# Kernel tuning notes

Measured on AMD Instinct MI355X. Metric: run time of the kernel, lower is better.

## Reference

```python
import jax, jax.numpy as jnp
from jax import lax
import numpy as np

NUM_CLASSES = 81
SCALES = (64.0, 128.0, 256.0)
RATIOS = (0.5, 1.0, 2.0)
A = 9                       # anchors per cell = len(SCALES)*len(RATIOS)
POOL = 14
PRE_NMS = 6000
PROPOSAL_COUNT = 1000
NMS_THR = 0.7
BN_EPS = 1e-3               # keras BatchNormalization default epsilon
NEG = -1e9                  # suppressed-score sentinel (avoids -inf NaNs in grad)


def conv(x, w, b, padding):
    return lax.conv_general_dilated(x, w, (1, 1), padding,
        dimension_numbers=('NHWC', 'HWIO', 'NHWC')) + b


def bn(x, g, b, m, v):
    # inference-mode batch norm
    return (x - m) * (g / jnp.sqrt(v + BN_EPS)) + b


def generate_anchors(fh, fw, H, W):
    sy, sx = H / fh, W / fw
    scales = jnp.asarray(SCALES, jnp.float32)
    sq = jnp.sqrt(jnp.asarray(RATIOS, jnp.float32))
    ah = (scales[:, None] * sq[None, :]).reshape(-1)   # [A]
    aw = (scales[:, None] / sq[None, :]).reshape(-1)
    cy = (jnp.arange(fh, dtype=jnp.float32) + 0.5) * sy
    cx = (jnp.arange(fw, dtype=jnp.float32) + 0.5) * sx
    cy, cx = jnp.meshgrid(cy, cx, indexing='ij')
    cy, cx = cy[..., None], cx[..., None]              # [fh,fw,1]
    # (y1, x1, y2, x2), flattened per-cell-then-anchor to match channel layout
    return jnp.stack([cy - ah / 2, cx - aw / 2, cy + ah / 2, cx + aw / 2], -1).reshape(-1, 4)


def decode(anchors, deltas):
    h = anchors[:, 2] - anchors[:, 0]
    w = anchors[:, 3] - anchors[:, 1]
    cy = anchors[:, 0] + 0.5 * h + deltas[:, 0] * h
    cx = anchors[:, 1] + 0.5 * w + deltas[:, 1] * w
    h = h * jnp.exp(deltas[:, 2])
    w = w * jnp.exp(deltas[:, 3])
    return jnp.stack([cy - 0.5 * h, cx - 0.5 * w, cy + 0.5 * h, cx + 0.5 * w], 1)


def iou_one_vs_all(box, boxes):
    y1 = jnp.maximum(box[0], boxes[:, 0]); x1 = jnp.maximum(box[1], boxes[:, 1])
    y2 = jnp.minimum(box[2], boxes[:, 2]); x2 = jnp.minimum(box[3], boxes[:, 3])
    inter = jnp.maximum(y2 - y1, 0.0) * jnp.maximum(x2 - x1, 0.0)
    a = (box[2] - box[0]) * (box[3] - box[1])
    b = (boxes[:, 2] - boxes[:, 0]) * (boxes[:, 3] - boxes[:, 1])
    return inter / (a + b - inter + 1e-8)


def nms(boxes, scores, max_out, thr):
    # greedy NMS with fixed iteration count (jit-friendly)
    def step(s, _):
        i = jnp.argmax(s)
        valid = s[i] > NEG * 0.5
        sup = iou_one_vs_all(boxes[i], boxes) > thr
        s = jnp.where(sup, NEG, s).at[i].set(NEG)
        return s, (i, valid)
    _, (idx, valid) = lax.scan(step, scores, None, length=max_out)
    return idx, valid


def roi_align(feat, boxes):
    # feat: [H, W, C]; boxes: [N, 4] normalized (y1, x1, y2, x2)
    H, W, _ = feat.shape
    t = jnp.arange(POOL, dtype=jnp.float32) / (POOL - 1)
    def one(box):
        y1, x1, y2, x2 = box
        ys = (y1 + t * (y2 - y1)) * (H - 1)
        xs = (x1 + t * (x2 - x1)) * (W - 1)
        y0 = jnp.clip(jnp.floor(ys), 0, H - 2).astype(jnp.int32)
        x0 = jnp.clip(jnp.floor(xs), 0, W - 2).astype(jnp.int32)
        wy = jnp.clip(ys - y0, 0.0, 1.0)[:, None, None]
        wx = jnp.clip(xs - x0, 0.0, 1.0)[None, :, None]
        r0, r1 = feat[y0], feat[y0 + 1]                    # [P, W, C]
        top = r0[:, x0] * (1 - wx) + r0[:, x0 + 1] * wx    # [P, P, C]
        bot = r1[:, x0] * (1 - wx) + r1[:, x0 + 1] * wx
        return top * (1 - wy) + bot * wy
    return jax.vmap(one)(boxes)                            # [N, P, P, C]


def setup_inputs() -> dict:
    key = jax.random.key(0)
    ks = jax.random.split(key, 12)
    f = lambda k, shp, s=0.02: jax.random.normal(k, shp, jnp.float32) * s
    C_in, C_fpn, C_rpn = 1024, 256, 512
    return dict(
        feature=jax.random.normal(ks[0], (1, 64, 64, C_in), jnp.float32),
        w_fpn1=f(ks[1], (1, 1, C_in, C_fpn)), b_fpn1=jnp.zeros((C_fpn,), jnp.float32),
        w_fpn2=f(ks[2], (3, 3, C_fpn, C_fpn)), b_fpn2=jnp.zeros((C_fpn,), jnp.float32),
        w_rpn=f(ks[3], (3, 3, C_fpn, C_rpn)), b_rpn=jnp.zeros((C_rpn,), jnp.float32),
        w_cls=f(ks[4], (1, 1, C_rpn, A * 2)), b_cls=jnp.zeros((A * 2,), jnp.float32),
        w_dlt=f(ks[5], (1, 1, C_rpn, A * 4)), b_dlt=jnp.zeros((A * 4,), jnp.float32),
        w_rc1=f(ks[6], (POOL, POOL, C_fpn, 1024), 0.005), b_rc1=jnp.zeros((1024,), jnp.float32),
        g1=jnp.ones((1024,), jnp.float32), be1=jnp.zeros((1024,), jnp.float32),
        m1=jnp.zeros((1024,), jnp.float32), v1=jnp.ones((1024,), jnp.float32),
        w_rc2=f(ks[7], (1024, 1024)), b_rc2=jnp.zeros((1024,), jnp.float32),
        g2=jnp.ones((1024,), jnp.float32), be2=jnp.zeros((1024,), jnp.float32),
        m2=jnp.zeros((1024,), jnp.float32), v2=jnp.ones((1024,), jnp.float32),
        w_log=f(ks[8], (1024, NUM_CLASSES)), b_log=jnp.zeros((NUM_CLASSES,), jnp.float32),
        w_bfc=f(ks[9], (1024, NUM_CLASSES * 4)), b_bfc=jnp.zeros((NUM_CLASSES * 4,), jnp.float32),
        image_h=512, image_w=512,
    )


def reference(feature, w_fpn1, b_fpn1, w_fpn2, b_fpn2, w_rpn, b_rpn, w_cls, b_cls,
              w_dlt, b_dlt, w_rc1, b_rc1, g1, be1, m1, v1, w_rc2, b_rc2, g2, be2,
              m2, v2, w_log, b_log, w_bfc, b_bfc, image_h, image_w):
    H, W = float(image_h), float(image_w)
    # ---- FPN neck: 1x1 then 3x3 conv to 256ch ----
    x = conv(feature, w_fpn1, b_fpn1, 'VALID')
    x = conv(x, w_fpn2, b_fpn2, 'SAME')                # [1, fh, fw, 256]
    fh, fw = x.shape[1], x.shape[2]
    # ---- RPN head ----
    shared = jax.nn.relu(conv(x, w_rpn, b_rpn, 'SAME'))
    rpn_logits = conv(shared, w_cls, b_cls, 'VALID').reshape(-1, 2)
    rpn_probs = jax.nn.softmax(rpn_logits, axis=-1)    # [num_anchors, 2]
    rpn_deltas = conv(shared, w_dlt, b_dlt, 'VALID').reshape(-1, 4)
    # ---- proposal generation: anchors -> top-k -> decode -> clip -> NMS ----
    anchors = generate_anchors(fh, fw, H, W)
    scores = rpn_probs[:, 1]
    k = min(PRE_NMS, anchors.shape[0])
    top_scores, ix = lax.top_k(scores, k)
    props = decode(anchors[ix], rpn_deltas[ix])
    window = jnp.asarray([H, W, H, W], jnp.float32)
    props = jnp.minimum(jnp.maximum(props, 0.0), window)   # bbox_clip
    props = props / window                                  # normalize
    sel, valid = nms(props, top_scores, PROPOSAL_COUNT, NMS_THR)
    proposals = props[sel] * valid[:, None].astype(props.dtype)  # [1000, 4]
    # ---- RoI pooling + RCNN head ----
    rois = roi_align(x[0], proposals)                       # [1000, 14, 14, 256]
    h1 = rois.reshape(PROPOSAL_COUNT, -1) @ w_rc1.reshape(-1, 1024) + b_rc1
    h1 = jax.nn.relu(bn(h1, g1, be1, m1, v1))
    h2 = jax.nn.relu(bn(h1 @ w_rc2 + b_rc2, g2, be2, m2, v2))
    cls_probs = jax.nn.softmax(h2 @ w_log + b_log, axis=-1)         # [1000, 81]
    box_deltas = (h2 @ w_bfc + b_bfc).reshape(-1, NUM_CLASSES, 4)   # [1000, 81, 4]
    return (rpn_probs.reshape(1, -1, 2), rpn_deltas.reshape(1, -1, 4),
            proposals, cls_probs, box_deltas)
```

## Files before the change

kernel.cpp:

```cpp
#include <hip/hip_runtime.h>
#include <hip/hip_bf16.h>

typedef unsigned int u32;
typedef unsigned long long u64;
typedef unsigned short u16;

typedef float f32x4 __attribute__((ext_vector_type(4)));
typedef __bf16 bf16x8 __attribute__((ext_vector_type(8)));
typedef unsigned short u16x8 __attribute__((ext_vector_type(8)));
typedef unsigned short u16x4 __attribute__((ext_vector_type(4)));

#define NA 36864
#define PRE_NMS 6000
#define NPROP 1000
#define KROI 50176
#define MASKW 94
#define MASKT_STRIDE 6144
#define KSPLIT 8
#define KCHUNK (KROI / KSPLIT)
#define BN_EPS 1e-3f
#define CONV_TILES 3136

__device__ __forceinline__ u16 f2bf(float v) {
    __bf16 h = (__bf16)v;
    return __builtin_bit_cast(u16, h);
}
__device__ __forceinline__ bf16x8 ldfrag(const u16* p) {
    return __builtin_bit_cast(bf16x8, *(const u16x8*)p);
}
__device__ __forceinline__ void gload16(const void* g, void* l) {
    __builtin_amdgcn_global_load_lds(
        (const __attribute__((address_space(1))) unsigned int*)g,
        (__attribute__((address_space(3))) unsigned int*)l, 16, 0, 0);
}

template <bool CONV3>
__global__ __launch_bounds__(128) void gemm_v3(
    const float* __restrict__ A, const float* __restrict__ B, float* __restrict__ part,
    int M, int N, int K, int kchunk) {
    __shared__ float As[2][16][132];
    __shared__ float Bs[2][16][68];
    const int tid = threadIdx.x;
    const int bm = blockIdx.x * 128, bn = blockIdx.y * 64;
    const int ks = blockIdx.z;
    const int kbeg = ks * kchunk, kend = kbeg + kchunk;
    const int tx = tid & 7, ty = tid >> 3;
    (void)K;

    float4 ra[4], rb[2];
    auto loadA = [&](int k0, int i) -> float4 {
        int e = tid + 128 * i;
        int m = e >> 2, kq = (e & 3) * 4;
        float4 v = {0.f, 0.f, 0.f, 0.f};
        int gm = bm + m;
        if (CONV3) {
            int gg = k0 >> 8;
            int dy = gg / 3, dx = gg - 3 * dy;
            int pr = gm >> 6, pc = gm & 63;
            int sr = pr + dy - 1, sc = pc + dx - 1;
            int ch = (k0 & 255) + kq;
            if (sr >= 0 && sr < 64 && sc >= 0 && sc < 64)
                v = *(const float4*)&A[(size_t)((sr << 6) + sc) * 256 + ch];
        } else {
            if (gm < M) v = *(const float4*)&A[(size_t)gm * K + k0 + kq];
        }
        return v;
    };
    auto loadB = [&](int k0, int i) -> float4 {
        int e = tid + 128 * i;
        int n4 = (e & 15) * 4, kk = e >> 4;
        return *(const float4*)&B[(size_t)(k0 + kk) * N + bn + n4];
    };
    auto stage = [&](int s) {
#pragma unroll
        for (int i = 0; i < 4; ++i) {
            int e = tid + 128 * i; int m = e >> 2, kq = (e & 3) * 4;
            As[s][kq + 0][m] = ra[i].x; As[s][kq + 1][m] = ra[i].y;
            As[s][kq + 2][m] = ra[i].z; As[s][kq + 3][m] = ra[i].w;
        }
#pragma unroll
        for (int i = 0; i < 2; ++i) {
            int e = tid + 128 * i; int n4 = (e & 15) * 4, kk = e >> 4;
            *(float4*)&Bs[s][kk][n4] = rb[i];
        }
    };

    float acc[8][8] = {};
#pragma unroll
    for (int i = 0; i < 4; ++i) ra[i] = loadA(kbeg, i);
#pragma unroll
    for (int i = 0; i < 2; ++i) rb[i] = loadB(kbeg, i);
    stage(0);
    if (kbeg + 16 < kend) {
#pragma unroll
        for (int i = 0; i < 4; ++i) ra[i] = loadA(kbeg + 16, i);
#pragma unroll
        for (int i = 0; i < 2; ++i) rb[i] = loadB(kbeg + 16, i);
    }
    __syncthreads();
    int s = 0;
    for (int k0 = kbeg; k0 < kend; k0 += 16) {
        if (k0 + 16 < kend) {
            stage(s ^ 1);
            if (k0 + 32 < kend) {
#pragma unroll
                for (int i = 0; i < 4; ++i) ra[i] = loadA(k0 + 32, i);
#pragma unroll
                for (int i = 0; i < 2; ++i) rb[i] = loadB(k0 + 32, i);
            }
        }
#pragma unroll
        for (int kk = 0; kk < 16; ++kk) {
            float4 a0 = *(const float4*)&As[s][kk][8 * ty];
            float4 a1 = *(const float4*)&As[s][kk][8 * ty + 4];
            float4 b0 = *(const float4*)&Bs[s][kk][8 * tx];
            float4 b1 = *(const float4*)&Bs[s][kk][8 * tx + 4];
            const float av[8] = {a0.x, a0.y, a0.z, a0.w, a1.x, a1.y, a1.z, a1.w};
            const float bv[8] = {b0.x, b0.y, b0.z, b0.w, b1.x, b1.y, b1.z, b1.w};
#pragma unroll
            for (int r = 0; r < 8; ++r)
#pragma unroll
                for (int c = 0; c < 8; ++c) acc[r][c] = fmaf(av[r], bv[c], acc[r][c]);
        }
        __syncthreads();
        s ^= 1;
    }
    float* P = part + (size_t)ks * ((size_t)M * N);
#pragma unroll
    for (int r = 0; r < 8; ++r) {
        int gm = bm + 8 * ty + r;
        if (gm >= M) continue;
        *(float4*)&P[(size_t)gm * N + bn + 8 * tx] = *(const float4*)&acc[r][0];
        *(float4*)&P[(size_t)gm * N + bn + 8 * tx + 4] = *(const float4*)&acc[r][4];
    }
}

template <int EPI>
__global__ __launch_bounds__(256) void reduce_part(
    const float* __restrict__ part, float* __restrict__ C, int M, int N, int KS,
    const float* __restrict__ bias, const float* __restrict__ g,
    const float* __restrict__ be, const float* __restrict__ mu,
    const float* __restrict__ var) {
    int i = blockIdx.x * 256 + threadIdx.x;
    int total = (M * N) >> 2;
    if (i >= total) return;
    size_t off = (size_t)i * 4;
    int n = (int)(off % (size_t)N);
    size_t slice = (size_t)M * N;
    float4 sv = {0.f, 0.f, 0.f, 0.f};
    for (int k = 0; k < KS; ++k) {
        float4 v = *(const float4*)&part[(size_t)k * slice + off];
        sv.x += v.x; sv.y += v.y; sv.z += v.z; sv.w += v.w;
    }
    float o[4] = {sv.x, sv.y, sv.z, sv.w};
#pragma unroll
    for (int j = 0; j < 4; ++j) {
        float v = o[j] + bias[n + j];
        if constexpr (EPI == 1) v = fmaxf(v, 0.f);
        if constexpr (EPI == 2) {
            float sc = g[n + j] / sqrtf(var[n + j] + BN_EPS);
            v = (v - mu[n + j]) * sc + be[n + j];
            v = fmaxf(v, 0.f);
        }
        o[j] = v;
    }
    *(float4*)&C[off] = *(const float4*)&o[0];
}

__global__ __launch_bounds__(256) void pack_heads(
    const float* __restrict__ wc, const float* __restrict__ wd,
    const float* __restrict__ bc, const float* __restrict__ bd,
    float* __restrict__ wCat, float* __restrict__ bCat) {
    int i = blockIdx.x * 256 + threadIdx.x;
    if (i < 512 * 64) {
        int k = i >> 6, n = i & 63;
        float v = 0.f;
        if (n < 18) v = wc[k * 18 + n];
        else if (n < 54) v = wd[k * 36 + (n - 18)];
        wCat[i] = v;
    }
    if (i < 64) bCat[i] = (i < 18) ? bc[i] : ((i < 54) ? bd[i - 18] : 0.f);
}

__global__ __launch_bounds__(256) void pack_roi_heads(
    const float* __restrict__ wl, const float* __restrict__ wb,
    const float* __restrict__ bl, const float* __restrict__ bb,
    float* __restrict__ wH, float* __restrict__ bH) {
    int i = blockIdx.x * 256 + threadIdx.x;
    if (i < 1024 * 512) {
        int k = i >> 9, n = i & 511;
        float v = 0.f;
        if (n < 81) v = wl[k * 81 + n];
        else if (n < 405) v = wb[k * 324 + (n - 81)];
        wH[i] = v;
    }
    if (i < 512) bH[i] = (i < 81) ? bl[i] : ((i < 405) ? bb[i - 81] : 0.f);
}

__global__ __launch_bounds__(256) void split_roi(
    const float* __restrict__ hr, float* __restrict__ out4) {
    int i = blockIdx.x * 256 + threadIdx.x;
    if (i >= NPROP * 324) return;
    int r = i / 324, c = i - r * 324;
    out4[i] = hr[r * 512 + 81 + c];
}

__global__ __launch_bounds__(256) void rpn_probs_keys(
    const float* __restrict__ hc, float* __restrict__ out0, float* __restrict__ out1,
    u64* __restrict__ keys) {
    int i = blockIdx.x * 256 + threadIdx.x;
    if (i >= NA) return;
    int cell = i / 9, a = i - cell * 9;
    const float* row = &hc[cell * 64];
    float l0 = row[2 * a], l1 = row[2 * a + 1];
    float m = fmaxf(l0, l1);
    float e0 = expf(l0 - m), e1 = expf(l1 - m);
    float ssum = e0 + e1;
    float p0 = e0 / ssum, p1 = e1 / ssum;
    out0[2 * i] = p0;
    out0[2 * i + 1] = p1;
    keys[i] = ((u64)__float_as_uint(p1) << 32) | (u64)(0xFFFFFFFFu - (u32)i);
    const float* src = row + 18 + 4 * a;
    float4 d = {src[0], src[1], src[2], src[3]};
    *(float4*)&out1[(size_t)i * 4] = d;
}

__global__ __launch_bounds__(1024) void radix_select_compact(
    const u64* __restrict__ keys, u64* __restrict__ skeys) {
    __shared__ u32 hist[256];
    __shared__ u64 sPrefix, sMask;
    __shared__ int sRank;
    __shared__ u32 sCount;
    int tid = threadIdx.x;
    if (tid == 0) { sPrefix = 0; sMask = 0; sRank = PRE_NMS; sCount = 0; }
    __syncthreads();
    for (int p = 56; p >= 0; p -= 8) {
        if (tid < 256) hist[tid] = 0;
        __syncthreads();
        u64 pref = sPrefix, msk = sMask;
        for (int i = tid; i < NA; i += 1024) {
            u64 k = keys[i];
            if ((k & msk) == pref) atomicAdd(&hist[(u32)((k >> p) & 255)], 1u);
        }
        __syncthreads();
        if (tid == 0) {
            int cum = 0, rank = sRank, sel = 0;
            for (int d = 255; d >= 0; --d) {
                int c = (int)hist[d];
                if (cum + c >= rank) { sel = d; sRank = rank - cum; break; }
                cum += c;
            }
            sPrefix = pref | ((u64)(u32)sel << p);
            sMask = msk | (0xFFull << p);
        }
        __syncthreads();
    }
    u64 thr = sPrefix;
    for (int i = tid; i < NA; i += 1024) {
        u64 k = keys[i];
        if (k >= thr) {
            u32 pos = atomicAdd(&sCount, 1u);
            skeys[pos] = k;
        }
    }
}

__global__ __launch_bounds__(256) void rank_decode(
    const u64* __restrict__ skeys, const float* __restrict__ deltas,
    const int* __restrict__ ih, const int* __restrict__ iw, float* __restrict__ props) {
    __shared__ u64 lds[PRE_NMS];
    const int tid = threadIdx.x;
    for (int i = tid; i < PRE_NMS; i += 256) lds[i] = skeys[i];
    __syncthreads();
    int i = blockIdx.x * 256 + tid;
    if (i >= PRE_NMS) return;
    u64 k = lds[i];
    int c = 0;
#pragma unroll 4
    for (int j = 0; j < PRE_NMS; ++j) c += (lds[j] > k) ? 1 : 0;
    u32 idx = 0xFFFFFFFFu - (u32)(k & 0xFFFFFFFFull);
    float H = (float)(*ih), W = (float)(*iw);
    int a = idx % 9;
    int cell = idx / 9;
    int r = cell >> 6, cc = cell & 63;
    float sy = H / 64.0f, sx = W / 64.0f;
    float cy = ((float)r + 0.5f) * sy, cx = ((float)cc + 0.5f) * sx;
    const float scales[3] = {64.f, 128.f, 256.f};
    const float ratios[3] = {0.5f, 1.f, 2.f};
    float sq = sqrtf(ratios[a % 3]);
    float scl = scales[a / 3];
    float ah = scl * sq, aw = scl / sq;
    float ay1 = cy - ah * 0.5f, ax1 = cx - aw * 0.5f;
    float h = ah, w = aw;
    float d0 = deltas[(size_t)idx * 4 + 0], d1 = deltas[(size_t)idx * 4 + 1];
    float d2 = deltas[(size_t)idx * 4 + 2], d3 = deltas[(size_t)idx * 4 + 3];
    float ncy = ay1 + 0.5f * h + d0 * h;
    float ncx = ax1 + 0.5f * w + d1 * w;
    float nh = h * expf(d2), nw = w * expf(d3);
    float y1 = ncy - 0.5f * nh, x1 = ncx - 0.5f * nw;
    float y2 = ncy + 0.5f * nh, x2 = ncx + 0.5f * nw;
    float4 box = {fminf(fmaxf(y1, 0.f), H) / H, fminf(fmaxf(x1, 0.f), W) / W,
                  fminf(fmaxf(y2, 0.f), H) / H, fminf(fmaxf(x2, 0.f), W) / W};
    *(float4*)&props[(size_t)c * 4] = box;
}

__global__ __launch_bounds__(256) void nms_masks(
    const float* __restrict__ props, u64* __restrict__ masksT, u64* __restrict__ diag) {
    __shared__ float4 chunk[64];
    int tid = threadIdx.x;
    int i = blockIdx.x * 256 + tid;
    int w = blockIdx.y;
    int jbase = w * 64;
    if (tid < 64 && jbase + tid < PRE_NMS)
        chunk[tid] = *(const float4*)&props[(size_t)(jbase + tid) * 4];
    __syncthreads();
    if (i >= PRE_NMS) return;
    float4 bi = *(const float4*)&props[(size_t)i * 4];
    float y1 = bi.x, x1 = bi.y, y2 = bi.z, x2 = bi.w;
    float ai = (y2 - y1) * (x2 - x1);
    u64 bits = 0;
    int lim = PRE_NMS - jbase; if (lim > 64) lim = 64;
    for (int b = 0; b < lim; ++b) {
        float4 bj = chunk[b];
        float iy1 = fmaxf(y1, bj.x), ix1 = fmaxf(x1, bj.y);
        float iy2 = fminf(y2, bj.z), ix2 = fminf(x2, bj.w);
        float inter = fmaxf(iy2 - iy1, 0.f) * fmaxf(ix2 - ix1, 0.f);
        float aj = (bj.z - bj.x) * (bj.w - bj.y);
        float iou = inter / (ai + aj - inter + 1e-8f);
        if (iou > 0.7f) bits |= (1ull << b);
    }
    masksT[(size_t)w * MASKT_STRIDE + i] = bits;
    if (w == (i >> 6)) diag[i] = bits;
}

__global__ __launch_bounds__(1024) void nms_greedy_conv(
    const u64* __restrict__ masksT, const u64* __restrict__ diag,
    const float* __restrict__ props, float* __restrict__ out2,
    const float* __restrict__ Wf, u16* __restrict__ WT) {
    __shared__ u64 sdiag[PRE_NMS];
    __shared__ int skept[NPROP];
    __shared__ u64 swpart[16];
    __shared__ int skcount;
    const int tid = threadIdx.x;

    if (blockIdx.x != 0) {
        u16* tile = (u16*)sdiag;
        int bid = blockIdx.x - 1;
        int kg = bid % 196, n0 = (bid / 196) * 64;
        int k0 = kg * 256;
        int kk = tid >> 4, n4 = (tid & 15) * 4;
        float4 v[4];
#pragma unroll
        for (int t = 0; t < 4; ++t)
            v[t] = *(const float4*)&Wf[(size_t)(k0 + t * 64 + kk) * 1024 + n0 + n4];
#pragma unroll
        for (int t = 0; t < 4; ++t) {
            u16* tt = tile + t * 64 * 68;
            tt[(n4 + 0) * 68 + kk] = f2bf(v[t].x);
            tt[(n4 + 1) * 68 + kk] = f2bf(v[t].y);
            tt[(n4 + 2) * 68 + kk] = f2bf(v[t].z);
            tt[(n4 + 3) * 68 + kk] = f2bf(v[t].w);
        }
        __syncthreads();
        int nn = tid >> 4, k4 = (tid & 15) * 4;
#pragma unroll
        for (int t = 0; t < 4; ++t) {
            u16x4 o = *(const u16x4*)&tile[(t * 64 + nn) * 68 + k4];
            *(u16x4*)&WT[(size_t)(n0 + nn) * KROI + k0 + t * 64 + k4] = o;
        }
        return;
    }

    const int lane = tid & 63;
    const int wid = tid >> 6;
    for (int i = tid; i < PRE_NMS; i += 1024) sdiag[i] = diag[i];
    if (tid == 0) skcount = 0;
    __syncthreads();
    int kept = 0;
    for (int c = 0; c < MASKW; ++c) {
        int keptNow = skcount;
        if (keptNow >= NPROP) break;
        u64 acc = 0;
        const u64* mrow = masksT + (size_t)c * MASKT_STRIDE;
        for (int t = tid; t < keptNow; t += 1024) acc |= mrow[skept[t]];
#pragma unroll
        for (int s = 32; s > 0; s >>= 1) acc |= __shfl_xor(acc, s);
        if (lane == 0) swpart[wid] = acc;
        __syncthreads();
        if (tid < 64) {
            u64 removed = 0;
#pragma unroll
            for (int q = 0; q < 16; ++q) removed |= swpart[q];
            int jbase = c * 64;
            int limit = PRE_NMS - jbase;
            u64 alive = ~removed;
            if (limit < 64) alive &= (1ull << limit) - 1ull;
            u64 mymask = (jbase + lane < PRE_NMS) ? sdiag[jbase + lane] : 0ull;
            while (alive && kept < NPROP) {
                int b = __ffsll((long long)alive) - 1;
                alive &= ~(1ull << b);
                u64 m = __shfl(mymask, b);
                if (lane == 0) skept[kept] = jbase + b;
                ++kept;
                alive &= ~m;
            }
            if (lane == 0) skcount = kept;
        }
        __syncthreads();
    }
    int keptFinal = skcount;
    for (int i = tid; i < NPROP * 4; i += 1024) {
        int p = i >> 2, d = i & 3;
        out2[i] = (p < keptFinal) ? props[(size_t)skept[p] * 4 + d] : 0.f;
    }
}

__global__ __launch_bounds__(256) void roi_align_k(
    const float* __restrict__ X2, const float* __restrict__ boxes, u16* __restrict__ rois) {
    int p = blockIdx.x;
    int c = threadIdx.x;
    float y1 = boxes[p * 4], x1 = boxes[p * 4 + 1], y2 = boxes[p * 4 + 2], x2 = boxes[p * 4 + 3];
    for (int py = 0; py < 14; ++py) {
        float ty = (float)py / 13.0f;
        float ys = (y1 + ty * (y2 - y1)) * 63.0f;
        float fy = fminf(fmaxf(floorf(ys), 0.f), 62.f);
        int y0 = (int)fy;
        float wy = fminf(fmaxf(ys - fy, 0.f), 1.f);
        for (int px = 0; px < 14; ++px) {
            float tx = (float)px / 13.0f;
            float xs = (x1 + tx * (x2 - x1)) * 63.0f;
            float fx = fminf(fmaxf(floorf(xs), 0.f), 62.f);
            int x0 = (int)fx;
            float wx = fminf(fmaxf(xs - fx, 0.f), 1.f);
            const float* r0 = X2 + (size_t)((y0) * 64 + x0) * 256 + c;
            const float* r1 = r0 + 64 * 256;
            float v00 = r0[0], v01 = r0[256];
            float v10 = r1[0], v11 = r1[256];
            float top = v00 * (1.f - wx) + v01 * wx;
            float bot = v10 * (1.f - wx) + v11 * wx;
            float v = top * (1.f - wy) + bot * wy;
            rois[((size_t)p * 196 + py * 14 + px) * 256 + c] = f2bf(v);
        }
    }
}

__global__ __launch_bounds__(256) void h1_gemm(
    const u16* __restrict__ Abf, const u16* __restrict__ Bbf, float* __restrict__ part) {
    const int tid = threadIdx.x;
    const int bid = blockIdx.x;
    const int ks = bid & 7;
    const int bm = ((bid >> 3) & 7) * 128;
    const int bn = (bid >> 6) * 128;
    __shared__ u16 As[128 * 64];
    __shared__ u16 Bs[128 * 64];
    const int wave = tid >> 6, lane = tid & 63;
    const size_t kbase = (size_t)ks * KCHUNK;
    const int wm = (wave >> 1) * 64, wn = (wave & 1) * 64;
    const int fr = lane & 15, fg = lane >> 4;
    const int srow = wave * 32 + (lane >> 3);
    const int scol = (((lane & 7) ^ (lane >> 3)) * 8);
    const size_t abase = (size_t)(bm + srow) * KROI + kbase + scol;
    const size_t bbase = (size_t)(bn + srow) * KROI + kbase + scol;
    u16* AsW = &As[wave * 2048];
    u16* BsW = &Bs[wave * 2048];

    f32x4 acc[4][4] = {};
    for (int k0 = 0; k0 < KCHUNK; k0 += 64) {
        __syncthreads();
#pragma unroll
        for (int i = 0; i < 4; ++i) {
            gload16(Abf + abase + (size_t)(i * 8) * KROI + k0, AsW + i * 512);
            gload16(Bbf + bbase + (size_t)(i * 8) * KROI + k0, BsW + i * 512);
        }
        __syncthreads();
        bf16x8 fa[4][2], fb[4][2];
#pragma unroll
        for (int t = 0; t < 4; ++t) {
#pragma unroll
            for (int s = 0; s < 2; ++s) {
                int ca = ((s * 4 + fg) ^ (fr & 7)) * 8;
                fa[t][s] = ldfrag(&As[(wm + t * 16 + fr) * 64 + ca]);
                fb[t][s] = ldfrag(&Bs[(wn + t * 16 + fr) * 64 + ca]);
            }
        }
#pragma unroll
        for (int s = 0; s < 2; ++s)
#pragma unroll
            for (int mi = 0; mi < 4; ++mi)
#pragma unroll
                for (int nj = 0; nj < 4; ++nj)
                    acc[mi][nj] = __builtin_amdgcn_mfma_f32_16x16x32_bf16(
                        fa[mi][s], fb[nj][s], acc[mi][nj], 0, 0, 0);
    }
    float* P = part + ((size_t)ks << 20);
#pragma unroll
    for (int mi = 0; mi < 4; ++mi) {
#pragma unroll
        for (int nj = 0; nj < 4; ++nj) {
            int r0 = bm + wm + mi * 16 + fg * 4;
            int c0 = bn + wn + nj * 16 + fr;
#pragma unroll
            for (int j = 0; j < 4; ++j)
                if (r0 + j < NPROP) P[(size_t)(r0 + j) * 1024 + c0] = acc[mi][nj][j];
        }
    }
}

__global__ __launch_bounds__(256) void reduce_h1(
    const float* __restrict__ part, const float* __restrict__ bias,
    const float* __restrict__ g, const float* __restrict__ be,
    const float* __restrict__ mu, const float* __restrict__ var, float* __restrict__ h1) {
    int i = blockIdx.x * 256 + threadIdx.x;
    if (i >= NPROP * 1024) return;
    int n = i & 1023, m = i >> 10;
    float s = 0.f;
#pragma unroll
    for (int k = 0; k < KSPLIT; ++k) s += part[((size_t)k << 20) + ((size_t)m << 10) + n];
    s += bias[n];
    float sc = g[n] / sqrtf(var[n] + BN_EPS);
    s = (s - mu[n]) * sc + be[n];
    h1[i] = fmaxf(s, 0.f);
}

__global__ __launch_bounds__(128) void softmax_cls(
    const float* __restrict__ hroi, float* __restrict__ out3) {
    __shared__ float sm[128];
    int row = blockIdx.x, t = threadIdx.x;
    float v = (t < 81) ? hroi[(size_t)row * 512 + t] : -1e30f;
    sm[t] = v;
    __syncthreads();
    for (int s = 64; s > 0; s >>= 1) {
        if (t < s) sm[t] = fmaxf(sm[t], sm[t + s]);
        __syncthreads();
    }
    float mx = sm[0];
    __syncthreads();
    float e = (t < 81) ? expf(v - mx) : 0.f;
    sm[t] = e;
    __syncthreads();
    for (int s = 64; s > 0; s >>= 1) {
        if (t < s) sm[t] += sm[t + s];
        __syncthreads();
    }
    float denom = sm[0];
    if (t < 81) out3[(size_t)row * 81 + t] = e / denom;
}

extern "C" void kernel_launch(void* const* d_in, const int* in_sizes, int n_in,
                              void* d_out, int out_size, void* d_ws, size_t ws_size,
                              hipStream_t stream) {
    const float* feature = (const float*)d_in[0];
    const float* w_fpn1 = (const float*)d_in[1];
    const float* b_fpn1 = (const float*)d_in[2];
    const float* w_fpn2 = (const float*)d_in[3];
    const float* b_fpn2 = (const float*)d_in[4];
    const float* w_rpn = (const float*)d_in[5];
    const float* b_rpn = (const float*)d_in[6];
    const float* w_cls = (const float*)d_in[7];
    const float* b_cls = (const float*)d_in[8];
    const float* w_dlt = (const float*)d_in[9];
    const float* b_dlt = (const float*)d_in[10];
    const float* w_rc1 = (const float*)d_in[11];
    const float* b_rc1 = (const float*)d_in[12];
    const float* g1 = (const float*)d_in[13];
    const float* be1 = (const float*)d_in[14];
    const float* m1 = (const float*)d_in[15];
    const float* v1 = (const float*)d_in[16];
    const float* w_rc2 = (const float*)d_in[17];
    const float* b_rc2 = (const float*)d_in[18];
    const float* g2 = (const float*)d_in[19];
    const float* be2 = (const float*)d_in[20];
    const float* m2 = (const float*)d_in[21];
    const float* v2 = (const float*)d_in[22];
    const float* w_log = (const float*)d_in[23];
    const float* b_log = (const float*)d_in[24];
    const float* w_bfc = (const float*)d_in[25];
    const float* b_bfc = (const float*)d_in[26];
    const int* image_h = (const int*)d_in[27];
    const int* image_w = (const int*)d_in[28];
    (void)in_sizes; (void)n_in; (void)out_size; (void)ws_size;

    float* out0 = (float*)d_out;
    float* out1 = out0 + 73728;
    float* out2 = out1 + 147456;
    float* out3 = out2 + 4000;
    float* out4 = out3 + 81000;

    char* wsb = (char*)d_ws;
    size_t off = 0;
    auto take = [&](size_t b) -> void* {
        off = (off + 255) & ~(size_t)255;
        void* p = wsb + off;
        off += b;
        return p;
    };
    float* x1 = (float*)take((size_t)4096 * 256 * 4);
    float* x2 = (float*)take((size_t)4096 * 256 * 4);
    float* shr = (float*)take((size_t)4096 * 512 * 4);
    float* hcat = (float*)take((size_t)4096 * 64 * 4);
    float* wCat = (float*)take((size_t)512 * 64 * 4);
    float* bCat = (float*)take((size_t)64 * 4);
    float* wHead = (float*)take((size_t)1024 * 512 * 4);
    float* bHead = (float*)take((size_t)512 * 4);
    float* hroi = (float*)take((size_t)NPROP * 512 * 4);
    u64* keys = (u64*)take((size_t)NA * 8);
    u64* skeys = (u64*)take((size_t)PRE_NMS * 8);
    float* props = (float*)take((size_t)PRE_NMS * 4 * 4);
    u64* masksT = (u64*)take((size_t)MASKW * MASKT_STRIDE * 8);
    u64* diag = (u64*)take((size_t)PRE_NMS * 8);
    u16* rois = (u16*)take((size_t)NPROP * KROI * 2);
    u16* wT = (u16*)take((size_t)1024 * KROI * 2);
    float* part = (float*)take((size_t)KSPLIT * 1024 * 1024 * 4);
    float* h1 = (float*)take((size_t)NPROP * 1024 * 4);
    float* h2 = (float*)take((size_t)NPROP * 1024 * 4);

    gemm_v3<false><<<dim3(32, 4, 8), 128, 0, stream>>>(feature, w_fpn1, part, 4096, 256, 1024, 128);
    reduce_part<0><<<dim3(1024), 256, 0, stream>>>(part, x1, 4096, 256, 8, b_fpn1, nullptr, nullptr, nullptr, nullptr);
    gemm_v3<true><<<dim3(32, 4, 8), 128, 0, stream>>>(x1, w_fpn2, part, 4096, 256, 2304, 288);
    reduce_part<0><<<dim3(1024), 256, 0, stream>>>(part, x2, 4096, 256, 8, b_fpn2, nullptr, nullptr, nullptr, nullptr);
    gemm_v3<true><<<dim3(32, 8, 4), 128, 0, stream>>>(x2, w_rpn, part, 4096, 512, 2304, 576);
    reduce_part<1><<<dim3(2048), 256, 0, stream>>>(part, shr, 4096, 512, 4, b_rpn, nullptr, nullptr, nullptr, nullptr);
    pack_heads<<<dim3(128), 256, 0, stream>>>(w_cls, w_dlt, b_cls, b_dlt, wCat, bCat);
    gemm_v3<false><<<dim3(32, 1, 8), 128, 0, stream>>>(shr, wCat, part, 4096, 64, 512, 64);
    reduce_part<0><<<dim3(256), 256, 0, stream>>>(part, hcat, 4096, 64, 8, bCat, nullptr, nullptr, nullptr, nullptr);
    rpn_probs_keys<<<dim3(144), 256, 0, stream>>>(hcat, out0, out1, keys);

    radix_select_compact<<<1, 1024, 0, stream>>>(keys, skeys);
    rank_decode<<<dim3(24), 256, 0, stream>>>(skeys, out1, image_h, image_w, props);
    nms_masks<<<dim3(24, 94), 256, 0, stream>>>(props, masksT, diag);
    nms_greedy_conv<<<dim3(1 + CONV_TILES), 1024, 0, stream>>>(masksT, diag, props, out2, w_rc1, wT);

    roi_align_k<<<dim3(1000), 256, 0, stream>>>(x2, out2, rois);
    h1_gemm<<<dim3(512), 256, 0, stream>>>(rois, wT, part);
    reduce_h1<<<dim3(4000), 256, 0, stream>>>(part, b_rc1, g1, be1, m1, v1, h1);
    gemm_v3<false><<<dim3(8, 16, 2), 128, 0, stream>>>(h1, w_rc2, part, 1000, 1024, 1024, 512);
    reduce_part<2><<<dim3(1000), 256, 0, stream>>>(part, h2, 1000, 1024, 2, b_rc2, g2, be2, m2, v2);
    pack_roi_heads<<<dim3(2048), 256, 0, stream>>>(w_log, w_bfc, b_log, b_bfc, wHead, bHead);
    gemm_v3<false><<<dim3(8, 8, 2), 128, 0, stream>>>(h2, wHead, part, 1000, 512, 1024, 512);
    reduce_part<0><<<dim3(500), 256, 0, stream>>>(part, hroi, 1000, 512, 2, bHead, nullptr, nullptr, nullptr, nullptr);
    split_roi<<<dim3(1266), 256, 0, stream>>>(hroi, out4);
    softmax_cls<<<dim3(1000), 128, 0, stream>>>(hroi, out3);
}
```

Before: 1.036 ms.

## Software-pipeline NMS mask reduction with greedy scan, one barrier per chunk

Restructures the single-block greedy NMS loop so waves 1-14 gather and OR the suppression masks for the next 64-box chunk while wave 0 runs the serial greedy scan on the current chunk. Wave 15 prefetches the masks from the previous chunk's boxes, and wave 0 folds them in using a kept-bit mask from the prior step. Results pass through double-buffered shared arrays, which cuts the barriers per chunk from two to one and takes the gather latency off the serial critical path. The cost is one fewer wave on the gather and more complex dependency handling across chunks.

```diff
diff --git a/kernel.cpp b/kernel.cpp
--- a/kernel.cpp
+++ b/kernel.cpp
@@ -339,8 +339,9 @@
     const float* __restrict__ Wf, u16* __restrict__ WT) {
     __shared__ u64 sdiag[PRE_NMS];
     __shared__ int skept[NPROP];
-    __shared__ u64 swpart[16];
-    __shared__ int skcount;
+    __shared__ u64 sG[2][16];
+    __shared__ u64 sP[2][64];
+    __shared__ int sBase;
     const int tid = threadIdx.x;
 
     if (blockIdx.x != 0) {
@@ -374,44 +375,64 @@
     const int lane = tid & 63;
     const int wid = tid >> 6;
     for (int i = tid; i < PRE_NMS; i += 1024) sdiag[i] = diag[i];
-    if (tid == 0) skcount = 0;
-    __syncthreads();
+    if (tid < 16) { sG[0][tid] = 0; sG[1][tid] = 0; }
+    if (tid < 64) { sP[0][tid] = 0; sP[1][tid] = 0; }
+    if (tid == 0) sBase = 0;
+    __syncthreads();
+
     int kept = 0;
+    u64 kbPrev = 0;
     for (int c = 0; c < MASKW; ++c) {
-        int keptNow = skcount;
-        if (keptNow >= NPROP) break;
-        u64 acc = 0;
-        const u64* mrow = masksT + (size_t)c * MASKT_STRIDE;
-        for (int t = tid; t < keptNow; t += 1024) acc |= mrow[skept[t]];
-#pragma unroll
-        for (int s = 32; s > 0; s >>= 1) acc |= __shfl_xor(acc, s);
-        if (lane == 0) swpart[wid] = acc;
-        __syncthreads();
-        if (tid < 64) {
-            u64 removed = 0;
-#pragma unroll
-            for (int q = 0; q < 16; ++q) removed |= swpart[q];
+        const int p = c & 1, q = p ^ 1;
+        int base = sBase;
+        if (base >= NPROP) break;
+
+        if (wid >= 1 && wid <= 14) {
+            u64 acc = 0;
+            if (c + 1 < MASKW) {
+                const u64* mrowN = masksT + (size_t)(c + 1) * MASKT_STRIDE;
+                for (int t = (wid - 1) * 64 + lane; t < base; t += 896)
+                    acc |= mrowN[skept[t]];
+            }
+#pragma unroll
+            for (int s = 32; s > 0; s >>= 1) acc |= __shfl_xor(acc, s);
+            if (lane == 0) sG[q][wid] = acc;
+        } else if (wid == 15) {
+            u64 v = 0;
+            int jb = c * 64;
+            if (c + 1 < MASKW && jb + lane < PRE_NMS)
+                v = masksT[(size_t)(c + 1) * MASKT_STRIDE + jb + lane];
+            sP[q][lane] = v;
+        } else {
+            u64 contrib = ((kbPrev >> lane) & 1ull) ? sP[p][lane] : 0ull;
+            if (lane >= 1 && lane <= 14) contrib |= sG[p][lane];
+#pragma unroll
+            for (int s = 32; s > 0; s >>= 1) contrib |= __shfl_xor(contrib, s);
+            u64 removed = contrib;
             int jbase = c * 64;
             int limit = PRE_NMS - jbase;
             u64 alive = ~removed;
             if (limit < 64) alive &= (1ull << limit) - 1ull;
             u64 mymask = (jbase + lane < PRE_NMS) ? sdiag[jbase + lane] : 0ull;
+            u64 kb = 0;
             while (alive && kept < NPROP) {
                 int b = __ffsll((long long)alive) - 1;
                 alive &= ~(1ull << b);
                 u64 m = __shfl(mymask, b);
                 if (lane == 0) skept[kept] = jbase + b;
                 ++kept;
+                kb |= (1ull << b);
                 alive &= ~m;
             }
-            if (lane == 0) skcount = kept;
-        }
-        __syncthreads();
-    }
-    int keptFinal = skcount;
+            kbPrev = kb;
+            if (lane == 0) sBase = kept;
+        }
+        __syncthreads();
+    }
+    int keptFinal = sBase;
     for (int i = tid; i < NPROP * 4; i += 1024) {
-        int p = i >> 2, d = i & 3;
-        out2[i] = (p < keptFinal) ? props[(size_t)skept[p] * 4 + d] : 0.f;
+        int pp = i >> 2, d = i & 3;
+        out2[i] = (pp < keptFinal) ? props[(size_t)skept[pp] * 4 + d] : 0.f;
     }
 }
 
```

After: 1.015 ms, median of 2. 1.02x faster.
